# Kernel tuning notes

Measured on AMD Instinct MI355X. Metric: run time of the kernel, lower is better.

## Reference

```python
import jax, jax.numpy as jnp
import numpy as np

N = 50000  # num nodes

def gcn_conv(x, edge_index, W, b, num_nodes):
    # x: [N, Fin] -> [N, Fout]; PyG GCNConv: linear, add self-loops, sym-norm aggregate, bias
    h = x @ W
    row, col = edge_index[0], edge_index[1]  # source j, target i
    loop = jnp.arange(num_nodes, dtype=row.dtype)
    row = jnp.concatenate([row, loop])
    col = jnp.concatenate([col, loop])
    deg = jax.ops.segment_sum(jnp.ones_like(col, dtype=h.dtype), col, num_segments=num_nodes)
    dinv = jnp.where(deg > 0, jax.lax.rsqrt(deg), 0.0)
    norm = dinv[row] * dinv[col]                      # [E+N]
    msg = h[row] * norm[:, None]                      # gather + scale
    out = jax.ops.segment_sum(msg, col, num_segments=num_nodes)
    return out + b

def setup_inputs() -> dict:
    key = jax.random.key(0)
    ks = jax.random.split(key, 8)
    F_in, H1, H2 = 128, 128, 64
    E_train, E_score = 600000, 200000
    x = jax.random.normal(ks[0], (N, F_in), dtype=jnp.float32)
    train_pos_edge_index = jax.random.randint(ks[1], (2, E_train), 0, N, dtype=jnp.int32)
    pos_edge_index = jax.random.randint(ks[2], (2, E_score), 0, N, dtype=jnp.int32)
    neg_edge_index = jax.random.randint(ks[3], (2, E_score), 0, N, dtype=jnp.int32)
    W1 = jax.random.normal(ks[4], (F_in, H1), dtype=jnp.float32) / np.sqrt(F_in)
    b1 = jnp.zeros((H1,), dtype=jnp.float32)
    W2 = jax.random.normal(ks[5], (H1, H2), dtype=jnp.float32) / np.sqrt(H1)
    b2 = jnp.zeros((H2,), dtype=jnp.float32)
    return {"x": x, "train_pos_edge_index": train_pos_edge_index,
            "pos_edge_index": pos_edge_index, "neg_edge_index": neg_edge_index,
            "W1": W1, "b1": b1, "W2": W2, "b2": b2}

def reference(x, train_pos_edge_index, pos_edge_index, neg_edge_index, W1, b1, W2, b2):
    h = jax.nn.relu(gcn_conv(x, train_pos_edge_index, W1, b1, N))
    h = gcn_conv(h, train_pos_edge_index, W2, b2, N)
    total = jnp.concatenate([pos_edge_index, neg_edge_index], axis=-1)  # [2, Ep+En]
    x_j = h[total[0]]
    x_i = h[total[1]]
    return jnp.einsum('ef,ef->e', x_i, x_j)
```

## Files before the change

### kernel.cpp

```cpp
#include <hip/hip_runtime.h>
#include <hip/hip_bf16.h>
#include <hip/hip_fp16.h>

#define NODES   50000
#define E_TRAIN 600000
#define E_SCORE 200000
#define CAP     48
#define G1B     782
#define CHUNK   2048
#define BINB    294
#define NB_C    391
#define SCAP    48
#define WTB     32

typedef unsigned short ushort_t;
typedef __attribute__((ext_vector_type(8))) short bf16x8;
typedef __attribute__((ext_vector_type(4))) float f32x4;

static __device__ __forceinline__ float bf2f(unsigned short u) {
    return __uint_as_float((unsigned int)u << 16);
}
static __device__ __forceinline__ unsigned short f2bf(float f) {
    __hip_bfloat16 h = __float2bfloat16(f);
    return *reinterpret_cast<unsigned short*>(&h);
}
static __device__ __forceinline__ unsigned short f2h(float f) {
    __half h = __float2half(f);
    return *reinterpret_cast<unsigned short*>(&h);
}
static __device__ __forceinline__ float2 u2f2(unsigned int u) {
    __half2 h = *reinterpret_cast<__half2*>(&u);
    return __half22float2(h);
}
static __device__ __forceinline__ unsigned int f22u(float a, float b) {
    __half2 h = __floats2half2_rn(a, b);
    return *reinterpret_cast<unsigned int*>(&h);
}
static __device__ __forceinline__ unsigned int f22u_bf(float a, float b) {
    return (unsigned int)f2bf(a) | ((unsigned int)f2bf(b) << 16);
}
static __device__ __forceinline__ bf16x8 cvt8(const float* p) {
    float4 v0 = *(const float4*)p;
    float4 v1 = *(const float4*)(p + 4);
    bf16x8 r;
    r[0] = (short)f2bf(v0.x); r[1] = (short)f2bf(v0.y);
    r[2] = (short)f2bf(v0.z); r[3] = (short)f2bf(v0.w);
    r[4] = (short)f2bf(v1.x); r[5] = (short)f2bf(v1.y);
    r[6] = (short)f2bf(v1.z); r[7] = (short)f2bf(v1.w);
    return r;
}

__global__ __launch_bounds__(256) void k13_bin_gemm1_w(
    const int* __restrict__ trow, const int* __restrict__ tcol,
    unsigned int* __restrict__ cbuf2, int* __restrict__ hcnt,
    const unsigned int* __restrict__ xw,
    const void* __restrict__ x, const void* __restrict__ W1,
    const void* __restrict__ b1, const void* __restrict__ W2,
    const void* __restrict__ b2,
    ushort_t* __restrict__ W2T, float* __restrict__ b1f, float* __restrict__ b2f,
    int* __restrict__ flag, ushort_t* __restrict__ g1)
{
    __shared__ __align__(16) int smi[8708];
    const int b = blockIdx.x, t = threadIdx.x;

    if (b < BINB) {
        int* cur = smi;
        for (int i = t; i < 512; i += 256) cur[i] = 0;
        __syncthreads();
        #pragma unroll
        for (int k = 0; k < 8; ++k) {
            int e = b * CHUNK + k * 256 + t;
            if (e < E_TRAIN) {
                unsigned int d = (unsigned int)tcol[e];
                unsigned int s = (unsigned int)trow[e];
                int bk = (int)(d >> 7);
                int slot = atomicAdd(&cur[bk], 1);
                if (slot < SCAP)
                    cbuf2[((size_t)bk * BINB + b) * SCAP + slot] = (d << 16) | s;
            }
        }
        __syncthreads();
        for (int i = t; i < NB_C; i += 256) hcnt[b * NB_C + i] = cur[i];
        return;
    }

    int* cvp = &smi[8704];
    if (t == 0) *cvp = 0;
    __syncthreads();
    {
        unsigned int wv = xw[t];
        int ex = ((wv & 0xFFFFu) >> 7) & 0xFF;
        if (ex >= 100 && ex <= 140) atomicAdd(cvp, 1);
    }
    __syncthreads();
    const bool isbf = *cvp >= 150;

    if (b < BINB + G1B) {
        ushort_t* wlds = (ushort_t*)smi;
        for (int idx = t; idx < 16384; idx += 256) {
            int k = idx >> 7, n = idx & 127;
            wlds[n * 136 + k] = isbf ? ((const ushort_t*)W1)[idx] : f2bf(((const float*)W1)[idx]);
        }
        __syncthreads();

        const int bb = b - BINB;
        const int lane = t & 63, wave = t >> 6;
        const int n = lane & 15, quad = lane >> 4;
        const int wr0 = bb * 64 + wave * 16;
        int rowA = wr0 + n; if (rowA > NODES - 1) rowA = NODES - 1;
        f32x4 acc[8];
        #pragma unroll
        for (int ct = 0; ct < 8; ++ct) acc[ct] = (f32x4){0.f, 0.f, 0.f, 0.f};
        #pragma unroll
        for (int kc = 0; kc < 4; ++kc) {
            bf16x8 a;
            if (isbf) a = *(const bf16x8*)((const ushort_t*)x + (long)rowA * 128 + kc * 32 + quad * 8);
            else      a = cvt8((const float*)x + (long)rowA * 128 + kc * 32 + quad * 8);
            #pragma unroll
            for (int ct = 0; ct < 8; ++ct) {
                bf16x8 bv = *(const bf16x8*)&wlds[(ct * 16 + n) * 136 + kc * 32 + quad * 8];
                acc[ct] = __builtin_amdgcn_mfma_f32_16x16x32_bf16(a, bv, acc[ct], 0, 0, 0);
            }
        }
        #pragma unroll
        for (int ct = 0; ct < 8; ++ct)
            #pragma unroll
            for (int r = 0; r < 4; ++r) {
                int orow = wr0 + quad * 4 + r;
                if (orow < NODES)
                    g1[(long)orow * 128 + ct * 16 + n] = f2h(acc[ct][r]);
            }
        return;
    }

    const int bw = b - BINB - G1B;
    if (bw == 0 && t == 0) flag[0] = isbf ? 1 : 0;
    int tid = bw * 256 + t;
    {
        int k = tid >> 6, n = tid & 63;
        W2T[n * 128 + k] = isbf ? ((const ushort_t*)W2)[tid] : f2bf(((const float*)W2)[tid]);
    }
    if (tid < 128) b1f[tid] = isbf ? bf2f(((const ushort_t*)b1)[tid]) : ((const float*)b1)[tid];
    if (tid < 64)  b2f[tid] = isbf ? bf2f(((const ushort_t*)b2)[tid]) : ((const float*)b2)[tid];
}

__global__ __launch_bounds__(256) void k2_fine(
    const unsigned int* __restrict__ cbuf2, const int* __restrict__ hcnt,
    int* __restrict__ esrc, int* __restrict__ cnt, float* __restrict__ dinvA)
{
    __shared__ int lcnt[128];
    __shared__ __align__(16) int lists[128 * CAP];
    const int bk = blockIdx.x, t = threadIdx.x;
    for (int i = t; i < 128; i += 256) lcnt[i] = 0;
    __syncthreads();
    const int st0 = t >> 1, sub = t & 1;
    for (int s0 = st0; s0 < BINB; s0 += 128) {
        int c = hcnt[s0 * NB_C + bk];
        if (c > SCAP) c = SCAP;
        const unsigned int* src = cbuf2 + ((size_t)bk * BINB + s0) * SCAP;
        for (int j = sub; j < c; j += 2) {
            unsigned int p = src[j];
            int fd = (int)((p >> 16) & 127);
            int s  = (int)(p & 0xFFFFu);
            int slot = atomicAdd(&lcnt[fd], 1);
            if (slot < CAP) lists[fd * CAP + slot] = s;
        }
    }
    __syncthreads();
    if (t < 128) {
        int d = bk * 128 + t;
        if (d < NODES) {
            int c = lcnt[t];
            cnt[d] = c;
            dinvA[d] = rsqrtf((float)c + 1.0f);
        }
    }
    const uint4* lv = (const uint4*)lists;
    uint4* ev = (uint4*)esrc;
    for (int i = t; i < 128 * CAP / 4; i += 256)
        ev[(long)bk * (128 * CAP / 4) + i] = lv[i];
}

__global__ __launch_bounds__(256) void k4_gather1_gemm2(
    const ushort_t* __restrict__ g1, const int* __restrict__ cnt,
    const float* __restrict__ dinvA,
    const int* __restrict__ esrc, const float* __restrict__ b1f,
    const ushort_t* __restrict__ W2T, ushort_t* __restrict__ g2)
{
    __shared__ ushort_t h1S[16 * 136];
    const int t = threadIdx.x;
    const int lane = t & 63, wave = t >> 6;
    const int quarter = lane >> 4, ql = lane & 15;
    const int d0 = blockIdx.x * 16;
    const int r = wave * 4 + quarter;
    const int d = d0 + r;
    const uint4* g1v = (const uint4*)g1;

    const int cdeg = cnt[d];
    const int m = cdeg < CAP ? cdeg : CAP;
    const int base = d * CAP;
    float a0=0.f,a1=0.f,a2=0.f,a3=0.f,a4=0.f,a5=0.f,a6=0.f,a7=0.f;
    int j = 0;
    for (; j + 2 <= m; j += 2) {
        int s0 = esrc[base + j], s1 = esrc[base + j + 1];
        float ds0 = dinvA[s0], ds1 = dinvA[s1];
        uint4 v0 = g1v[(long)s0 * 16 + ql];
        uint4 v1 = g1v[(long)s1 * 16 + ql];
        float2 p;
        p = u2f2(v0.x); a0 = fmaf(p.x, ds0, a0); a1 = fmaf(p.y, ds0, a1);
        p = u2f2(v0.y); a2 = fmaf(p.x, ds0, a2); a3 = fmaf(p.y, ds0, a3);
        p = u2f2(v0.z); a4 = fmaf(p.x, ds0, a4); a5 = fmaf(p.y, ds0, a5);
        p = u2f2(v0.w); a6 = fmaf(p.x, ds0, a6); a7 = fmaf(p.y, ds0, a7);
        p = u2f2(v1.x); a0 = fmaf(p.x, ds1, a0); a1 = fmaf(p.y, ds1, a1);
        p = u2f2(v1.y); a2 = fmaf(p.x, ds1, a2); a3 = fmaf(p.y, ds1, a3);
        p = u2f2(v1.z); a4 = fmaf(p.x, ds1, a4); a5 = fmaf(p.y, ds1, a5);
        p = u2f2(v1.w); a6 = fmaf(p.x, ds1, a6); a7 = fmaf(p.y, ds1, a7);
    }
    if (j < m) {
        int s0 = esrc[base + j];
        float ds0 = dinvA[s0];
        uint4 v0 = g1v[(long)s0 * 16 + ql];
        float2 p;
        p = u2f2(v0.x); a0 = fmaf(p.x, ds0, a0); a1 = fmaf(p.y, ds0, a1);
        p = u2f2(v0.y); a2 = fmaf(p.x, ds0, a2); a3 = fmaf(p.y, ds0, a3);
        p = u2f2(v0.z); a4 = fmaf(p.x, ds0, a4); a5 = fmaf(p.y, ds0, a5);
        p = u2f2(v0.w); a6 = fmaf(p.x, ds0, a6); a7 = fmaf(p.y, ds0, a7);
    }
    float dd = dinvA[d];
    uint4 gv = g1v[(long)d * 16 + ql];
    float4 bA = *(const float4*)(b1f + ql * 8);
    float4 bB = *(const float4*)(b1f + ql * 8 + 4);
    float2 p;
    p = u2f2(gv.x); float w0 = fmaxf(dd * (a0 + dd * p.x) + bA.x, 0.f), w1 = fmaxf(dd * (a1 + dd * p.y) + bA.y, 0.f);
    p = u2f2(gv.y); float w2 = fmaxf(dd * (a2 + dd * p.x) + bA.z, 0.f), w3 = fmaxf(dd * (a3 + dd * p.y) + bA.w, 0.f);
    p = u2f2(gv.z); float w4 = fmaxf(dd * (a4 + dd * p.x) + bB.x, 0.f), w5 = fmaxf(dd * (a5 + dd * p.y) + bB.y, 0.f);
    p = u2f2(gv.w); float w6 = fmaxf(dd * (a6 + dd * p.x) + bB.z, 0.f), w7 = fmaxf(dd * (a7 + dd * p.y) + bB.w, 0.f);
    {
        uint4 ov;
        ov.x = f22u_bf(w0, w1); ov.y = f22u_bf(w2, w3);
        ov.z = f22u_bf(w4, w5); ov.w = f22u_bf(w6, w7);
        *(uint4*)&h1S[r * 136 + ql * 8] = ov;
    }
    __syncthreads();

    const int n = lane & 15, quad = lane >> 4;
    f32x4 acc = (f32x4){0.f, 0.f, 0.f, 0.f};
    #pragma unroll
    for (int kc = 0; kc < 4; ++kc) {
        bf16x8 a = *(const bf16x8*)&h1S[n * 136 + kc * 32 + quad * 8];
        bf16x8 bv = *(const bf16x8*)(W2T + (wave * 16 + n) * 128 + kc * 32 + quad * 8);
        acc = __builtin_amdgcn_mfma_f32_16x16x32_bf16(a, bv, acc, 0, 0, 0);
    }
    __syncthreads();
    #pragma unroll
    for (int rr = 0; rr < 4; ++rr) {
        int drow = quad * 4 + rr;
        float sc = dinvA[d0 + drow];
        h1S[drow * 72 + wave * 16 + n] = f2h(acc[rr] * sc);
    }
    __syncthreads();
    if (t < 128) {
        int row = t >> 3, cir = t & 7;
        *(uint4*)&g2[((long)d0 + row) * 64 + cir * 8] = *(const uint4*)&h1S[row * 72 + cir * 8];
    }
}

__global__ __launch_bounds__(256) void k5_gather2(
    const ushort_t* __restrict__ g2, const int* __restrict__ cnt,
    const float* __restrict__ dinvA,
    const int* __restrict__ esrc, const float* __restrict__ b2f,
    unsigned int* __restrict__ h2)
{
    const int t = threadIdx.x;
    const int lane = t & 63, wave = t >> 6;
    const int oct = lane >> 3, ol = lane & 7;
    const int d = blockIdx.x * 32 + wave * 8 + oct;
    if (d >= NODES) return;
    const uint4* g2v = (const uint4*)g2;

    const int cdeg = cnt[d];
    const int m = cdeg < CAP ? cdeg : CAP;
    const int base = d * CAP;
    float a0=0.f,a1=0.f,a2=0.f,a3=0.f,a4=0.f,a5=0.f,a6=0.f,a7=0.f;
    int j = 0;
    for (; j + 2 <= m; j += 2) {
        int s0 = esrc[base + j], s1 = esrc[base + j + 1];
        uint4 v0 = g2v[(long)s0 * 8 + ol];
        uint4 v1 = g2v[(long)s1 * 8 + ol];
        float2 p;
        p = u2f2(v0.x); a0 += p.x; a1 += p.y;
        p = u2f2(v0.y); a2 += p.x; a3 += p.y;
        p = u2f2(v0.z); a4 += p.x; a5 += p.y;
        p = u2f2(v0.w); a6 += p.x; a7 += p.y;
        p = u2f2(v1.x); a0 += p.x; a1 += p.y;
        p = u2f2(v1.y); a2 += p.x; a3 += p.y;
        p = u2f2(v1.z); a4 += p.x; a5 += p.y;
        p = u2f2(v1.w); a6 += p.x; a7 += p.y;
    }
    if (j < m) {
        uint4 v0 = g2v[(long)esrc[base + j] * 8 + ol];
        float2 p;
        p = u2f2(v0.x); a0 += p.x; a1 += p.y;
        p = u2f2(v0.y); a2 += p.x; a3 += p.y;
        p = u2f2(v0.z); a4 += p.x; a5 += p.y;
        p = u2f2(v0.w); a6 += p.x; a7 += p.y;
    }
    float dd = dinvA[d];
    uint4 gv = g2v[(long)d * 8 + ol];
    float4 bA = *(const float4*)(b2f + ol * 8);
    float4 bB = *(const float4*)(b2f + ol * 8 + 4);
    float2 p0 = u2f2(gv.x), p1 = u2f2(gv.y), p2 = u2f2(gv.z), p3 = u2f2(gv.w);
    uint4 ov;
    ov.x = f22u(dd * (a0 + p0.x) + bA.x, dd * (a1 + p0.y) + bA.y);
    ov.y = f22u(dd * (a2 + p1.x) + bA.z, dd * (a3 + p1.y) + bA.w);
    ov.z = f22u(dd * (a4 + p2.x) + bB.x, dd * (a5 + p2.y) + bB.y);
    ov.w = f22u(dd * (a6 + p3.x) + bB.z, dd * (a7 + p3.y) + bB.w);
    *(uint4*)&h2[(long)d * 32 + ol * 4] = ov;
}

__global__ __launch_bounds__(256) void k6_score(
    const int* __restrict__ pos, const int* __restrict__ neg,
    const unsigned int* __restrict__ h2, void* __restrict__ out,
    const int* __restrict__ flag)
{
    int e = blockIdx.x * 256 + threadIdx.x;
    if (e >= 2 * E_SCORE) return;
    int s, d;
    if (e < E_SCORE) { s = pos[e];           d = pos[E_SCORE + e]; }
    else             { int i = e - E_SCORE; s = neg[i]; d = neg[E_SCORE + i]; }
    const uint4* A = (const uint4*)(h2 + (long)s * 32);
    const uint4* B = (const uint4*)(h2 + (long)d * 32);
    float acc = 0.f;
    #pragma unroll
    for (int q = 0; q < 8; ++q) {
        uint4 ua = A[q], ub = B[q];
        float2 a0 = u2f2(ua.x), b0 = u2f2(ub.x);
        float2 a1 = u2f2(ua.y), b1 = u2f2(ub.y);
        float2 a2 = u2f2(ua.z), b2 = u2f2(ub.z);
        float2 a3 = u2f2(ua.w), b3 = u2f2(ub.w);
        acc += a0.x * b0.x + a0.y * b0.y + a1.x * b1.x + a1.y * b1.y
             + a2.x * b2.x + a2.y * b2.y + a3.x * b3.x + a3.y * b3.y;
    }
    if (flag[0]) ((ushort_t*)out)[e] = f2bf(acc);
    else         ((float*)out)[e] = acc;
}

extern "C" void kernel_launch(void* const* d_in, const int* in_sizes, int n_in,
                              void* d_out, int out_size, void* d_ws, size_t ws_size,
                              hipStream_t stream) {
    const void* x      = d_in[0];
    const int*  etrain = (const int*)d_in[1];
    const int*  pos    = (const int*)d_in[2];
    const int*  neg    = (const int*)d_in[3];
    const void* W1     = d_in[4];
    const void* b1     = d_in[5];
    const void* W2     = d_in[6];
    const void* b2     = d_in[7];

    char* ws = (char*)d_ws;
    int*          flag   = (int*)(ws + 0);
    int*          cnt    = (int*)(ws + 256);
    float*        dinvA  = (float*)(ws + 200448);
    ushort_t*     W2T    = (ushort_t*)(ws + 400640);
    float*        b1f    = (float*)(ws + 417024);
    float*        b2f    = (float*)(ws + 417536);
    int*          hcnt   = (int*)(ws + 417792);
    int*          esrc   = (int*)(ws + 877824);
    unsigned int* cbuf2  = (unsigned int*)(ws + 10487040);
    ushort_t*     g1     = (ushort_t*)(ws + 32558208);
    ushort_t*     g2     = (ushort_t*)(ws + 45358208);
    unsigned int* h2     = (unsigned int*)(ws + 51758208);

    const int* trow = etrain;
    const int* tcol = etrain + E_TRAIN;


    k13_bin_gemm1_w<<<BINB + G1B + WTB, 256, 0, stream>>>(
        trow, tcol, cbuf2, hcnt, (const unsigned int*)x,
        x, W1, b1, W2, b2, W2T, b1f, b2f, flag, g1);

    k2_fine<<<NB_C, 256, 0, stream>>>(cbuf2, hcnt, esrc, cnt, dinvA);

    k4_gather1_gemm2<<<3125, 256, 0, stream>>>(g1, cnt, dinvA, esrc, b1f, W2T, g2);

    k5_gather2<<<1563, 256, 0, stream>>>(g2, cnt, dinvA, esrc, b2f, h2);

    k6_score<<<1563, 256, 0, stream>>>(pos, neg, h2, d_out, flag);
}
```

Before: 187.6 us.

## Transpose bin buffer layout, swizzle W1 LDS, unroll gathers by four

The binning stage now writes each source block's bucket lists contiguously, and the per-bucket counts are stored transposed so the fine pass reads them contiguously. The W1 tile in LDS uses an XOR swizzle on 8-element chunks to reduce bank conflicts on MFMA operand loads. Both gather kernels unroll neighbor accumulation by four, reading the neighbor indices as one int4 load to expose more outstanding memory requests. The int4 load relies on the per-node list base (d*CAP) being 16-byte aligned, which holds because CAP is 48. Unrolling by four raises register pressure.

```diff
diff --git a/kernel.cpp b/kernel.cpp
--- a/kernel.cpp
+++ b/kernel.cpp
@@ -52,7 +52,7 @@
 
 __global__ __launch_bounds__(256) void k13_bin_gemm1_w(
     const int* __restrict__ trow, const int* __restrict__ tcol,
-    unsigned int* __restrict__ cbuf2, int* __restrict__ hcnt,
+    unsigned int* __restrict__ cbuf2, int* __restrict__ hcntT,
     const unsigned int* __restrict__ xw,
     const void* __restrict__ x, const void* __restrict__ W1,
     const void* __restrict__ b1, const void* __restrict__ W2,
@@ -67,6 +67,7 @@
         int* cur = smi;
         for (int i = t; i < 512; i += 256) cur[i] = 0;
         __syncthreads();
+        unsigned int* my = cbuf2 + (size_t)b * (NB_C * SCAP);
         #pragma unroll
         for (int k = 0; k < 8; ++k) {
             int e = b * CHUNK + k * 256 + t;
@@ -76,11 +77,11 @@
                 int bk = (int)(d >> 7);
                 int slot = atomicAdd(&cur[bk], 1);
                 if (slot < SCAP)
-                    cbuf2[((size_t)bk * BINB + b) * SCAP + slot] = (d << 16) | s;
+                    my[bk * SCAP + slot] = (d << 16) | s;
             }
         }
         __syncthreads();
-        for (int i = t; i < NB_C; i += 256) hcnt[b * NB_C + i] = cur[i];
+        for (int i = t; i < NB_C; i += 256) hcntT[i * BINB + b] = cur[i];
         return;
     }
 
@@ -99,7 +100,8 @@
         ushort_t* wlds = (ushort_t*)smi;
         for (int idx = t; idx < 16384; idx += 256) {
             int k = idx >> 7, n = idx & 127;
-            wlds[n * 136 + k] = isbf ? ((const ushort_t*)W1)[idx] : f2bf(((const float*)W1)[idx]);
+            int pos = n * 136 + ((((k >> 3) ^ (n & 7)) << 3) | (k & 7));
+            wlds[pos] = isbf ? ((const ushort_t*)W1)[idx] : f2bf(((const float*)W1)[idx]);
         }
         __syncthreads();
 
@@ -118,7 +120,9 @@
             else      a = cvt8((const float*)x + (long)rowA * 128 + kc * 32 + quad * 8);
             #pragma unroll
             for (int ct = 0; ct < 8; ++ct) {
-                bf16x8 bv = *(const bf16x8*)&wlds[(ct * 16 + n) * 136 + kc * 32 + quad * 8];
+                int row = ct * 16 + n;
+                int chk = ((kc << 2) | quad) ^ (n & 7);
+                bf16x8 bv = *(const bf16x8*)&wlds[row * 136 + (chk << 3)];
                 acc[ct] = __builtin_amdgcn_mfma_f32_16x16x32_bf16(a, bv, acc[ct], 0, 0, 0);
             }
         }
@@ -145,7 +149,7 @@
 }
 
 __global__ __launch_bounds__(256) void k2_fine(
-    const unsigned int* __restrict__ cbuf2, const int* __restrict__ hcnt,
+    const unsigned int* __restrict__ cbuf2, const int* __restrict__ hcntT,
     int* __restrict__ esrc, int* __restrict__ cnt, float* __restrict__ dinvA)
 {
     __shared__ int lcnt[128];
@@ -155,9 +159,9 @@
     __syncthreads();
     const int st0 = t >> 1, sub = t & 1;
     for (int s0 = st0; s0 < BINB; s0 += 128) {
-        int c = hcnt[s0 * NB_C + bk];
+        int c = hcntT[bk * BINB + s0];
         if (c > SCAP) c = SCAP;
-        const unsigned int* src = cbuf2 + ((size_t)bk * BINB + s0) * SCAP;
+        const unsigned int* src = cbuf2 + ((size_t)s0 * NB_C + bk) * SCAP;
         for (int j = sub; j < c; j += 2) {
             unsigned int p = src[j];
             int fd = (int)((p >> 16) & 127);
@@ -201,11 +205,13 @@
     const int base = d * CAP;
     float a0=0.f,a1=0.f,a2=0.f,a3=0.f,a4=0.f,a5=0.f,a6=0.f,a7=0.f;
     int j = 0;
-    for (; j + 2 <= m; j += 2) {
-        int s0 = esrc[base + j], s1 = esrc[base + j + 1];
-        float ds0 = dinvA[s0], ds1 = dinvA[s1];
-        uint4 v0 = g1v[(long)s0 * 16 + ql];
-        uint4 v1 = g1v[(long)s1 * 16 + ql];
+    for (; j + 4 <= m; j += 4) {
+        int4 s4 = *(const int4*)&esrc[base + j];
+        float ds0 = dinvA[s4.x], ds1 = dinvA[s4.y], ds2 = dinvA[s4.z], ds3 = dinvA[s4.w];
+        uint4 v0 = g1v[(long)s4.x * 16 + ql];
+        uint4 v1 = g1v[(long)s4.y * 16 + ql];
+        uint4 v2 = g1v[(long)s4.z * 16 + ql];
+        uint4 v3 = g1v[(long)s4.w * 16 + ql];
         float2 p;
         p = u2f2(v0.x); a0 = fmaf(p.x, ds0, a0); a1 = fmaf(p.y, ds0, a1);
         p = u2f2(v0.y); a2 = fmaf(p.x, ds0, a2); a3 = fmaf(p.y, ds0, a3);
@@ -215,8 +221,16 @@
         p = u2f2(v1.y); a2 = fmaf(p.x, ds1, a2); a3 = fmaf(p.y, ds1, a3);
         p = u2f2(v1.z); a4 = fmaf(p.x, ds1, a4); a5 = fmaf(p.y, ds1, a5);
         p = u2f2(v1.w); a6 = fmaf(p.x, ds1, a6); a7 = fmaf(p.y, ds1, a7);
-    }
-    if (j < m) {
+        p = u2f2(v2.x); a0 = fmaf(p.x, ds2, a0); a1 = fmaf(p.y, ds2, a1);
+        p = u2f2(v2.y); a2 = fmaf(p.x, ds2, a2); a3 = fmaf(p.y, ds2, a3);
+        p = u2f2(v2.z); a4 = fmaf(p.x, ds2, a4); a5 = fmaf(p.y, ds2, a5);
+        p = u2f2(v2.w); a6 = fmaf(p.x, ds2, a6); a7 = fmaf(p.y, ds2, a7);
+        p = u2f2(v3.x); a0 = fmaf(p.x, ds3, a0); a1 = fmaf(p.y, ds3, a1);
+        p = u2f2(v3.y); a2 = fmaf(p.x, ds3, a2); a3 = fmaf(p.y, ds3, a3);
+        p = u2f2(v3.z); a4 = fmaf(p.x, ds3, a4); a5 = fmaf(p.y, ds3, a5);
+        p = u2f2(v3.w); a6 = fmaf(p.x, ds3, a6); a7 = fmaf(p.y, ds3, a7);
+    }
+    for (; j < m; ++j) {
         int s0 = esrc[base + j];
         float ds0 = dinvA[s0];
         uint4 v0 = g1v[(long)s0 * 16 + ql];
@@ -283,10 +297,12 @@
     const int base = d * CAP;
     float a0=0.f,a1=0.f,a2=0.f,a3=0.f,a4=0.f,a5=0.f,a6=0.f,a7=0.f;
     int j = 0;
-    for (; j + 2 <= m; j += 2) {
-        int s0 = esrc[base + j], s1 = esrc[base + j + 1];
-        uint4 v0 = g2v[(long)s0 * 8 + ol];
-        uint4 v1 = g2v[(long)s1 * 8 + ol];
+    for (; j + 4 <= m; j += 4) {
+        int4 s4 = *(const int4*)&esrc[base + j];
+        uint4 v0 = g2v[(long)s4.x * 8 + ol];
+        uint4 v1 = g2v[(long)s4.y * 8 + ol];
+        uint4 v2 = g2v[(long)s4.z * 8 + ol];
+        uint4 v3 = g2v[(long)s4.w * 8 + ol];
         float2 p;
         p = u2f2(v0.x); a0 += p.x; a1 += p.y;
         p = u2f2(v0.y); a2 += p.x; a3 += p.y;
@@ -296,8 +312,16 @@
         p = u2f2(v1.y); a2 += p.x; a3 += p.y;
         p = u2f2(v1.z); a4 += p.x; a5 += p.y;
         p = u2f2(v1.w); a6 += p.x; a7 += p.y;
-    }
-    if (j < m) {
+        p = u2f2(v2.x); a0 += p.x; a1 += p.y;
+        p = u2f2(v2.y); a2 += p.x; a3 += p.y;
+        p = u2f2(v2.z); a4 += p.x; a5 += p.y;
+        p = u2f2(v2.w); a6 += p.x; a7 += p.y;
+        p = u2f2(v3.x); a0 += p.x; a1 += p.y;
+        p = u2f2(v3.y); a2 += p.x; a3 += p.y;
+        p = u2f2(v3.z); a4 += p.x; a5 += p.y;
+        p = u2f2(v3.w); a6 += p.x; a7 += p.y;
+    }
+    for (; j < m; ++j) {
         uint4 v0 = g2v[(long)esrc[base + j] * 8 + ol];
         float2 p;
         p = u2f2(v0.x); a0 += p.x; a1 += p.y;
@@ -364,7 +388,7 @@
     ushort_t*     W2T    = (ushort_t*)(ws + 400640);
     float*        b1f    = (float*)(ws + 417024);
     float*        b2f    = (float*)(ws + 417536);
-    int*          hcnt   = (int*)(ws + 417792);
+    int*          hcntT  = (int*)(ws + 417792);
     int*          esrc   = (int*)(ws + 877824);
     unsigned int* cbuf2  = (unsigned int*)(ws + 10487040);
     ushort_t*     g1     = (ushort_t*)(ws + 32558208);
@@ -374,12 +398,11 @@
     const int* trow = etrain;
     const int* tcol = etrain + E_TRAIN;
 
-
     k13_bin_gemm1_w<<<BINB + G1B + WTB, 256, 0, stream>>>(
-        trow, tcol, cbuf2, hcnt, (const unsigned int*)x,
+        trow, tcol, cbuf2, hcntT, (const unsigned int*)x,
         x, W1, b1, W2, b2, W2T, b1f, b2f, flag, g1);
 
-    k2_fine<<<NB_C, 256, 0, stream>>>(cbuf2, hcnt, esrc, cnt, dinvA);
+    k2_fine<<<NB_C, 256, 0, stream>>>(cbuf2, hcntT, esrc, cnt, dinvA);
 
     k4_gather1_gemm2<<<3125, 256, 0, stream>>>(g1, cnt, dinvA, esrc, b1f, W2T, g2);
 
```

Measured after the change: 187.2 us. No clear change (-0.2%).
